# Kernel optimization log

Hardware: AMD Instinct MI355X
Metric: run time of the kernel (lower is better)

## Reference

```python
import jax, jax.numpy as jnp
import numpy as np

B, N, C, H, R = 64, 197, 768, 12, 24  # batch, tokens (196 patches + cls), dim, heads, lora rank
D = C // H  # head_dim = 64


def make_rel_index(ws=(14, 14)):
    Wh, Ww = ws
    coords = np.stack(np.meshgrid(np.arange(Wh), np.arange(Ww), indexing='ij'))  # [2,Wh,Ww]
    cf = coords.reshape(2, -1)
    rel = (cf[:, :, None] - cf[:, None, :]).transpose(1, 2, 0).astype(np.int64)
    rel[:, :, 0] += Wh - 1
    rel[:, :, 1] += Ww - 1
    rel[:, :, 0] *= 2 * Ww - 1
    num_rel = (2 * Wh - 1) * (2 * Ww - 1) + 3
    idx = np.zeros((Wh * Ww + 1,) * 2, dtype=np.int32)
    idx[1:, 1:] = rel.sum(-1)
    idx[0, :] = num_rel - 3
    idx[:, 0] = num_rel - 2
    idx[0, 0] = num_rel - 1
    return idx


def setup_inputs() -> dict:
    key = jax.random.key(0)
    ks = jax.random.split(key, 16)
    s = 0.02
    # 1D rotary table over 196 patch positions, interleaved pairs over head_dim
    pos = np.arange(N - 1, dtype=np.float32)
    inv_freq = 1.0 / (10000.0 ** (np.arange(0, D, 2, dtype=np.float32) / D))  # [D/2]
    ang = np.repeat(pos[:, None] * inv_freq[None, :], 2, axis=-1)  # [196, 64]
    return {
        'x': jax.random.normal(ks[0], (B, N, C), jnp.float32),
        'qkv_w': jax.random.normal(ks[1], (3 * C, C), jnp.float32) * s,
        'q_bias': jax.random.normal(ks[2], (C,), jnp.float32) * s,
        'v_bias': jax.random.normal(ks[3], (C,), jnp.float32) * s,
        'lora_q_a': jax.random.normal(ks[4], (R, C), jnp.float32) * s,
        'lora_q_b': jax.random.normal(ks[5], (C, R), jnp.float32) * s,
        'lora_k_a': jax.random.normal(ks[6], (R, C), jnp.float32) * s,
        'lora_k_b': jax.random.normal(ks[7], (C, R), jnp.float32) * s,
        'lora_v_a': jax.random.normal(ks[8], (R, C), jnp.float32) * s,
        'lora_v_b': jax.random.normal(ks[9], (C, R), jnp.float32) * s,
        'rel_table': jax.random.normal(ks[10], (732, H), jnp.float32) * s,
        'rope_cos': jnp.asarray(np.cos(ang)),
        'rope_sin': jnp.asarray(np.sin(ang)),
        'proj_w': jax.random.normal(ks[11], (C, C), jnp.float32) * s,
        'proj_b': jax.random.normal(ks[12], (C,), jnp.float32) * s,
        'rel_index': jnp.asarray(make_rel_index((14, 14))),
    }


def _rope(t, cos, sin):
    # t: [B,H,M,D]; cos/sin: [M,D]; EVA rotate_half over interleaved pairs
    tp = t.reshape(t.shape[:-1] + (D // 2, 2))
    rot = jnp.stack((-tp[..., 1], tp[..., 0]), axis=-1).reshape(t.shape)
    return t * cos + rot * sin


def reference(x, qkv_w, q_bias, v_bias, lora_q_a, lora_q_b, lora_k_a, lora_k_b,
              lora_v_a, lora_v_b, rel_table, rope_cos, rope_sin, proj_w, proj_b, rel_index):
    b, n, c = x.shape
    h = rel_table.shape[1]
    d = c // h
    scale = d ** -0.5
    bias = jnp.concatenate([q_bias, jnp.zeros_like(v_bias), v_bias])
    qkv = x @ qkv_w.T + bias  # [B,N,3C]
    lora = jnp.concatenate([(x @ lora_q_a.T) @ lora_q_b.T,
                            (x @ lora_k_a.T) @ lora_k_b.T,
                            (x @ lora_v_a.T) @ lora_v_b.T], axis=-1)
    qkv = (qkv + lora).reshape(b, n, 3, h, d).transpose(2, 0, 3, 1, 4)  # [3,B,H,N,D]
    q, k, v = qkv[0], qkv[1], qkv[2]
    # rope on non-cls tokens only
    q = jnp.concatenate([q[:, :, :1], _rope(q[:, :, 1:], rope_cos, rope_sin)], axis=2)
    k = jnp.concatenate([k[:, :, :1], _rope(k[:, :, 1:], rope_cos, rope_sin)], axis=2)
    attn = jnp.einsum('bhqd,bhkd->bhqk', (q * scale).astype(jnp.float32), k.astype(jnp.float32))
    rpb = rel_table[rel_index.reshape(-1)].reshape(n, n, h).transpose(2, 0, 1)  # [H,N,N]
    attn = attn + rpb[None].astype(attn.dtype)
    attn = jax.nn.softmax(attn, axis=-1).astype(x.dtype)
    out = jnp.einsum('bhqk,bhkd->bhqd', attn, v).transpose(0, 2, 1, 3).reshape(b, n, c)
    return out @ proj_w.T + proj_b
```

## Files before the change

### kernel.cpp

```cpp
#include <hip/hip_runtime.h>
#include <stdint.h>

typedef __bf16 bf16x8 __attribute__((ext_vector_type(8)));
typedef short short8 __attribute__((ext_vector_type(8)));
typedef float f32x4 __attribute__((ext_vector_type(4)));
typedef float f32x4v __attribute__((ext_vector_type(4)));
typedef unsigned short u16x4 __attribute__((ext_vector_type(4)));

#define DEV static __device__ __forceinline__

DEV float b2f(unsigned short u) {
    union { float f; unsigned v; } x; x.v = ((unsigned)u) << 16; return x.f;
}
DEV unsigned short f2b(float f) {
    union { float f; unsigned v; } x; x.f = f;
    unsigned r = x.v + 0x7fffu + ((x.v >> 16) & 1u);
    return (unsigned short)(r >> 16);
}
DEV f32x4 zero4() { f32x4 z; z[0]=0.f; z[1]=0.f; z[2]=0.f; z[3]=0.f; return z; }

#define MFMA16(a, b, c) __builtin_amdgcn_mfma_f32_16x16x32_bf16(a, b, c, 0, 0, 0)

DEV void gload16(const unsigned short* g, unsigned short* l) {
    __builtin_amdgcn_global_load_lds(
        (const __attribute__((address_space(1))) void*)g,
        (__attribute__((address_space(3))) void*)l,
        16, 0, 0);
}

__global__ __launch_bounds__(256)
void prep_kernel(const float* __restrict__ x, unsigned short* __restrict__ xb,
                 const float* __restrict__ pw, unsigned short* __restrict__ pwb,
                 const float* __restrict__ qkvw,
                 const float* __restrict__ qa, const float* __restrict__ qbb,
                 const float* __restrict__ ka, const float* __restrict__ kb,
                 const float* __restrict__ va, const float* __restrict__ vbb,
                 unsigned short* __restrict__ W,
                 const float* __restrict__ rtab, const int* __restrict__ ridx,
                 float* __restrict__ rpb)
{
    const int S0 = 9682944 / 4;
    const int S1 = 589824 / 4;
    const int S2 = 2304 * 768;
    const int S3 = 12 * 197 * 224;
    const int total = S0 + S1 + S2 + S3;
    for (int i = blockIdx.x * 256 + threadIdx.x; i < total; i += gridDim.x * 256) {
        if (i < S0) {
            f32x4v v = *(const f32x4v*)(x + (size_t)i * 4);
            u16x4 o;
            #pragma unroll
            for (int j = 0; j < 4; ++j) o[j] = f2b(v[j]);
            *(u16x4*)(xb + (size_t)i * 4) = o;
        } else if (i < S0 + S1) {
            const int k = i - S0;
            f32x4v v = *(const f32x4v*)(pw + (size_t)k * 4);
            u16x4 o;
            #pragma unroll
            for (int j = 0; j < 4; ++j) o[j] = f2b(v[j]);
            *(u16x4*)(pwb + (size_t)k * 4) = o;
        } else if (i < S0 + S1 + S2) {
            const int idx = i - S0 - S1;
            const int o = idx / 768;
            const int c = idx - o * 768;
            const int sec = o / 768;
            const int ol = o - sec * 768;
            const float* a_ = (sec == 0) ? qa : (sec == 1 ? ka : va);
            const float* b_ = (sec == 0) ? qbb : (sec == 1 ? kb : vbb);
            float acc = qkvw[idx];
            #pragma unroll
            for (int r = 0; r < 24; ++r)
                acc += b_[ol * 24 + r] * a_[r * 768 + c];
            W[idx] = f2b(acc);
        } else {
            const int idx = i - S0 - S1 - S2;
            const int h = idx / (197 * 224);
            const int rem = idx - h * 197 * 224;
            const int qq = rem / 224;
            const int kk = rem - qq * 224;
            float v = 0.f;
            if (kk < 197) v = rtab[ridx[qq * 197 + kk] * 12 + h];
            rpb[idx] = v;
        }
    }
}

template<int EPI>
__global__ __launch_bounds__(256, 2)
void gemm_bt(const unsigned short* __restrict__ A, const unsigned short* __restrict__ Bw,
             int M, int Nout, int ntn,
             const float* __restrict__ qb, const float* __restrict__ vb,
             const float* __restrict__ rcos, const float* __restrict__ rsin,
             unsigned short* __restrict__ oq, unsigned short* __restrict__ ok,
             unsigned short* __restrict__ ov,
             const float* __restrict__ pb, float* __restrict__ o2)
{
    constexpr int K = 768, TK = 24;
    __shared__ __align__(16) unsigned short lA[3][128 * 32];
    __shared__ __align__(16) unsigned short lB[3][128 * 32];
    const int tid = threadIdx.x;
    const int lane = tid & 63, wave = tid >> 6;

    const int nwg = gridDim.x;
    const int qq_ = nwg >> 3, rr_ = nwg & 7;
    const int xcd = blockIdx.x & 7, orig8 = blockIdx.x >> 3;
    const int wgid = (xcd < rr_ ? xcd * (qq_ + 1) : rr_ * (qq_ + 1) + (xcd - rr_) * qq_) + orig8;
    const int mt = wgid / ntn, nt = wgid - mt * ntn;
    const int m0 = mt * 128, n0 = nt * 128;
    const int wm = (wave >> 1) * 64, wn = (wave & 1) * 64;

    int srow[2], sunit[2];
    #pragma unroll
    for (int j = 0; j < 2; ++j) {
        const int P = wave * 2048 + j * 1024 + lane * 16;
        const int L = P ^ (((P >> 7) & 7) << 4);
        srow[j] = L >> 6;
        sunit[j] = (L >> 4) & 3;
    }

    const int laneA = lane & 15, laneQ = lane >> 4;
    int aoff[4], boff[4];
    #pragma unroll
    for (int i = 0; i < 4; ++i) {
        int lb = (wm + i * 16 + laneA) * 64 + laneQ * 16;
        aoff[i] = (lb ^ (((lb >> 7) & 7) << 4)) >> 1;
        lb = (wn + i * 16 + laneA) * 64 + laneQ * 16;
        boff[i] = (lb ^ (((lb >> 7) & 7) << 4)) >> 1;
    }

    f32x4 acc[4][4];
    #pragma unroll
    for (int i = 0; i < 4; ++i)
        #pragma unroll
        for (int j = 0; j < 4; ++j) acc[i][j] = zero4();

    auto stage = [&](int kt, int bsel) {
        const int k0 = kt << 5;
        #pragma unroll
        for (int j = 0; j < 2; ++j) {
            int gr = m0 + srow[j]; if (gr > M - 1) gr = M - 1;
            gload16(A + (size_t)gr * K + k0 + sunit[j] * 8,
                    (unsigned short*)lA[bsel] + wave * 1024 + j * 512);
        }
        #pragma unroll
        for (int j = 0; j < 2; ++j) {
            const int br = n0 + srow[j];
            gload16(Bw + (size_t)br * K + k0 + sunit[j] * 8,
                    (unsigned short*)lB[bsel] + wave * 1024 + j * 512);
        }
    };

    stage(0, 0);
    stage(1, 1);
    asm volatile("s_waitcnt vmcnt(4)" ::: "memory");
    __builtin_amdgcn_s_barrier();

    #pragma unroll
    for (int t = 0; t < TK; ++t) {
        if (t + 2 < TK) stage(t + 2, (t + 2) % 3);
        const unsigned short* aT = (const unsigned short*)lA[t % 3];
        const unsigned short* bT = (const unsigned short*)lB[t % 3];
        bf16x8 af[4], bfr[4];
        #pragma unroll
        for (int i = 0; i < 4; ++i) af[i] = *(const bf16x8*)(aT + aoff[i]);
        #pragma unroll
        for (int i = 0; i < 4; ++i) bfr[i] = *(const bf16x8*)(bT + boff[i]);
        #pragma unroll
        for (int mi = 0; mi < 4; ++mi)
            #pragma unroll
            for (int ni = 0; ni < 4; ++ni)
                acc[mi][ni] = MFMA16(af[mi], bfr[ni], acc[mi][ni]);
        if (t + 1 < TK) {
            if (t + 2 < TK) asm volatile("s_waitcnt vmcnt(4)" ::: "memory");
            else            asm volatile("s_waitcnt vmcnt(0)" ::: "memory");
            __builtin_amdgcn_s_barrier();
        }
    }

    #pragma unroll
    for (int mi = 0; mi < 4; ++mi) {
        #pragma unroll
        for (int j = 0; j < 4; ++j) {
            const int m = m0 + wm + mi * 16 + (lane >> 4) * 4 + j;
            const bool mv = (m < M);
            int b_ = 0, n = 0;
            if constexpr (EPI == 1) { b_ = m / 197; n = m - b_ * 197; }
            #pragma unroll
            for (int ni = 0; ni < 4; ++ni) {
                const int o = n0 + wn + ni * 16 + laneA;
                float val = acc[mi][ni][j];
                if constexpr (EPI == 1) {
                    const int sec = o / 768;
                    const int oc = o - sec * 768;
                    const int d = oc & 63;
                    if (sec == 0) val += qb[oc];
                    else if (sec == 2) val += vb[oc];
                    if (sec < 2 && n > 0) {
                        const float part = __shfl_xor(val, 1, 64);
                        const float co = rcos[(n - 1) * 64 + d];
                        const float si = rsin[(n - 1) * 64 + d];
                        val = val * co + ((o & 1) ? part : -part) * si;
                    }
                    if (sec == 0) val *= 0.125f;
                    if (mv) {
                        const int h = oc >> 6;
                        unsigned short* dst = (sec == 0) ? oq : (sec == 1 ? ok : ov);
                        dst[((size_t)(b_ * 12 + h) * 197 + n) * 64 + d] = f2b(val);
                    }
                } else {
                    val += pb[o];
                    if (mv) o2[(size_t)m * Nout + o] = val;
                }
            }
        }
    }
}

__global__ __launch_bounds__(256)
void attn_kernel(const unsigned short* __restrict__ qs, const unsigned short* __restrict__ ksrc,
                 const unsigned short* __restrict__ vsrc, const float* __restrict__ rpb,
                 unsigned short* __restrict__ aout)
{
    __shared__ __align__(16) unsigned short Pl[64 * 232];
    __shared__ __align__(16) unsigned short Vt[64 * 232];
    __shared__ float inv_s[64];
    const int chunk = blockIdx.x;
    const int h = blockIdx.y;
    const int b = blockIdx.z;
    const int tid = threadIdx.x, lane = tid & 63, wave = tid >> 6;
    const size_t base = ((size_t)(b * 12 + h)) * 197 * 64;
    const unsigned short* q = qs + base;
    const unsigned short* kp = ksrc + base;
    const unsigned short* vp = vsrc + base;

    if (tid < 224) {
        const int kc = tid;
        if (kc < 197) {
            #pragma unroll
            for (int d0 = 0; d0 < 8; ++d0) {
                short8 vv = *(const short8*)(vp + kc * 64 + d0 * 8);
                #pragma unroll
                for (int i = 0; i < 8; ++i)
                    Vt[(d0 * 8 + i) * 232 + kc] = (unsigned short)vv[i];
            }
        } else {
            #pragma unroll
            for (int dd = 0; dd < 64; ++dd) Vt[dd * 232 + kc] = 0;
        }
    }

    const int laneA = lane & 15;
    const int laneK = (lane >> 4) * 8;
    const int q0 = chunk * 64 + wave * 16;

    int qr = q0 + laneA; if (qr > 196) qr = 196;
    const bf16x8 qf0 = *(const bf16x8*)(q + qr * 64 + laneK);
    const bf16x8 qf1 = *(const bf16x8*)(q + qr * 64 + 32 + laneK);

    f32x4 s[13];
    #pragma unroll
    for (int kt = 0; kt < 13; ++kt) {
        int kr = kt * 16 + laneA; if (kr > 196) kr = 196;
        const bf16x8 kf0 = *(const bf16x8*)(kp + kr * 64 + laneK);
        const bf16x8 kf1 = *(const bf16x8*)(kp + kr * 64 + 32 + laneK);
        f32x4 c = zero4();
        c = MFMA16(qf0, kf0, c);
        c = MFMA16(qf1, kf1, c);
        s[kt] = c;
    }

    const int rowb = (lane >> 4) * 4;
    float mx[4] = {-1e30f, -1e30f, -1e30f, -1e30f};
    #pragma unroll
    for (int kt = 0; kt < 13; ++kt) {
        const int kc = kt * 16 + laneA;
        #pragma unroll
        for (int j = 0; j < 4; ++j) {
            int qg = q0 + rowb + j; if (qg > 196) qg = 196;
            float v = s[kt][j] + rpb[((size_t)h * 197 + qg) * 224 + kc];
            if (kc > 196) v = -1e30f;
            s[kt][j] = v;
            mx[j] = fmaxf(mx[j], v);
        }
    }
    #pragma unroll
    for (int off = 1; off < 16; off <<= 1)
        #pragma unroll
        for (int j = 0; j < 4; ++j) mx[j] = fmaxf(mx[j], __shfl_xor(mx[j], off, 64));
    float sm[4] = {0.f, 0.f, 0.f, 0.f};
    #pragma unroll
    for (int kt = 0; kt < 13; ++kt)
        #pragma unroll
        for (int j = 0; j < 4; ++j) {
            const float e = __expf(s[kt][j] - mx[j]);
            s[kt][j] = e;
            sm[j] += e;
        }
    #pragma unroll
    for (int off = 1; off < 16; off <<= 1)
        #pragma unroll
        for (int j = 0; j < 4; ++j) sm[j] += __shfl_xor(sm[j], off, 64);
    if (laneA == 0) {
        #pragma unroll
        for (int j = 0; j < 4; ++j) inv_s[wave * 16 + rowb + j] = 1.0f / sm[j];
    }
    #pragma unroll
    for (int kt = 0; kt < 13; ++kt) {
        const int kc = kt * 16 + laneA;
        #pragma unroll
        for (int j = 0; j < 4; ++j) {
            const int lr = wave * 16 + rowb + j;
            Pl[lr * 232 + kc] = (kc <= 196) ? f2b(s[kt][j]) : (unsigned short)0;
        }
    }
    #pragma unroll
    for (int j = 0; j < 4; ++j)
        Pl[(wave * 16 + rowb + j) * 232 + 208 + laneA] = 0;

    __syncthreads();

    f32x4 oacc[4];
    #pragma unroll
    for (int i = 0; i < 4; ++i) oacc[i] = zero4();
    #pragma unroll
    for (int ks2 = 0; ks2 < 7; ++ks2) {
        const bf16x8 pf = *(const bf16x8*)(Pl + (wave * 16 + laneA) * 232 + ks2 * 32 + laneK);
        #pragma unroll
        for (int ni = 0; ni < 4; ++ni) {
            const bf16x8 vf = *(const bf16x8*)(Vt + (ni * 16 + laneA) * 232 + ks2 * 32 + laneK);
            oacc[ni] = MFMA16(pf, vf, oacc[ni]);
        }
    }
    #pragma unroll
    for (int ni = 0; ni < 4; ++ni)
        #pragma unroll
        for (int j = 0; j < 4; ++j) {
            const int lq = wave * 16 + rowb + j;
            const int qg = chunk * 64 + lq;
            if (qg < 197) {
                const int d = ni * 16 + laneA;
                const float val = oacc[ni][j] * inv_s[lq];
                aout[((size_t)b * 197 + qg) * 768 + h * 64 + d] = f2b(val);
            }
        }
}

extern "C" void kernel_launch(void* const* d_in, const int* in_sizes, int n_in,
                              void* d_out, int out_size, void* d_ws, size_t ws_size,
                              hipStream_t stream)
{
    const float* x    = (const float*)d_in[0];
    const float* qkvw = (const float*)d_in[1];
    const float* qb   = (const float*)d_in[2];
    const float* vb   = (const float*)d_in[3];
    const float* lqa  = (const float*)d_in[4];
    const float* lqb  = (const float*)d_in[5];
    const float* lka  = (const float*)d_in[6];
    const float* lkb  = (const float*)d_in[7];
    const float* lva  = (const float*)d_in[8];
    const float* lvb  = (const float*)d_in[9];
    const float* rtab = (const float*)d_in[10];
    const float* rcos = (const float*)d_in[11];
    const float* rsin = (const float*)d_in[12];
    const float* pw   = (const float*)d_in[13];
    const float* pb   = (const float*)d_in[14];
    const int* ridx   = (const int*)d_in[15];

    const int M = 64 * 197;
    const size_t XSZ = (size_t)M * 768;
    const size_t QSZ = (size_t)64 * 12 * 197 * 64;

    char* ws = (char*)d_ws;
    unsigned short* xb   = (unsigned short*)ws;
    unsigned short* pwb  = xb + XSZ;
    unsigned short* Weff = pwb + (size_t)768 * 768;
    unsigned short* qsb  = Weff + (size_t)2304 * 768;
    unsigned short* ksb  = qsb + QSZ;
    unsigned short* vsb  = ksb + QSZ;
    float* rpb           = (float*)(vsb + QSZ);
    unsigned short* aout = (unsigned short*)(rpb + (size_t)12 * 197 * 224);

    prep_kernel<<<2048, 256, 0, stream>>>(x, xb, pw, pwb, qkvw,
                                          lqa, lqb, lka, lkb, lva, lvb, Weff,
                                          rtab, ridx, rpb);
    gemm_bt<1><<<99 * 18, 256, 0, stream>>>(xb, Weff, M, 2304, 18,
                                            qb, vb, rcos, rsin, qsb, ksb, vsb,
                                            nullptr, nullptr);
    attn_kernel<<<dim3(4, 12, 64), 256, 0, stream>>>(qsb, ksb, vsb, rpb, aout);
    gemm_bt<2><<<99 * 6, 256, 0, stream>>>(aout, pwb, M, 768, 6,
                                           nullptr, nullptr, nullptr, nullptr,
                                           nullptr, nullptr, nullptr,
                                           pb, (float*)d_out);
}
```

Baseline: 239.8 us.

## Replace LDS-staged GEMM with direct global-to-register double-buffered loads

Both projection GEMMs now skip shared memory entirely. Each lane loads its MFMA operand fragments straight from global memory into a two-deep register buffer, and the launch bound rises to allow three blocks per CU. This removes the LDS staging, swizzle math and per-step barriers. In exchange, operand rows are re-read by multiple waves instead of being shared through LDS, which raises cache and global traffic and gives less coalesced access.

```diff
diff --git a/kernel.cpp b/kernel.cpp
--- a/kernel.cpp
+++ b/kernel.cpp
@@ -20,13 +20,6 @@
 DEV f32x4 zero4() { f32x4 z; z[0]=0.f; z[1]=0.f; z[2]=0.f; z[3]=0.f; return z; }
 
 #define MFMA16(a, b, c) __builtin_amdgcn_mfma_f32_16x16x32_bf16(a, b, c, 0, 0, 0)
-
-DEV void gload16(const unsigned short* g, unsigned short* l) {
-    __builtin_amdgcn_global_load_lds(
-        (const __attribute__((address_space(1))) void*)g,
-        (__attribute__((address_space(3))) void*)l,
-        16, 0, 0);
-}
 
 __global__ __launch_bounds__(256)
 void prep_kernel(const float* __restrict__ x, unsigned short* __restrict__ xb,
@@ -85,18 +78,16 @@
 }
 
 template<int EPI>
-__global__ __launch_bounds__(256, 2)
-void gemm_bt(const unsigned short* __restrict__ A, const unsigned short* __restrict__ Bw,
-             int M, int Nout, int ntn,
-             const float* __restrict__ qb, const float* __restrict__ vb,
-             const float* __restrict__ rcos, const float* __restrict__ rsin,
-             unsigned short* __restrict__ oq, unsigned short* __restrict__ ok,
-             unsigned short* __restrict__ ov,
-             const float* __restrict__ pb, float* __restrict__ o2)
+__global__ __launch_bounds__(256, 3)
+void gemm_nolds(const unsigned short* __restrict__ A, const unsigned short* __restrict__ Bw,
+                int M, int Nout, int ntn,
+                const float* __restrict__ qb, const float* __restrict__ vb,
+                const float* __restrict__ rcos, const float* __restrict__ rsin,
+                unsigned short* __restrict__ oq, unsigned short* __restrict__ ok,
+                unsigned short* __restrict__ ov,
+                const float* __restrict__ pb, float* __restrict__ o2)
 {
     constexpr int K = 768, TK = 24;
-    __shared__ __align__(16) unsigned short lA[3][128 * 32];
-    __shared__ __align__(16) unsigned short lB[3][128 * 32];
     const int tid = threadIdx.x;
     const int lane = tid & 63, wave = tid >> 6;
 
@@ -108,23 +99,19 @@
     const int m0 = mt * 128, n0 = nt * 128;
     const int wm = (wave >> 1) * 64, wn = (wave & 1) * 64;
 
-    int srow[2], sunit[2];
-    #pragma unroll
-    for (int j = 0; j < 2; ++j) {
-        const int P = wave * 2048 + j * 1024 + lane * 16;
-        const int L = P ^ (((P >> 7) & 7) << 4);
-        srow[j] = L >> 6;
-        sunit[j] = (L >> 4) & 3;
-    }
-
     const int laneA = lane & 15, laneQ = lane >> 4;
-    int aoff[4], boff[4];
+
+    const unsigned short* ap[4];
+    const unsigned short* bp[4];
     #pragma unroll
     for (int i = 0; i < 4; ++i) {
-        int lb = (wm + i * 16 + laneA) * 64 + laneQ * 16;
-        aoff[i] = (lb ^ (((lb >> 7) & 7) << 4)) >> 1;
-        lb = (wn + i * 16 + laneA) * 64 + laneQ * 16;
-        boff[i] = (lb ^ (((lb >> 7) & 7) << 4)) >> 1;
+        int ar = m0 + wm + i * 16 + laneA; if (ar > M - 1) ar = M - 1;
+        ap[i] = A + (size_t)ar * K + laneQ * 8;
+    }
+    #pragma unroll
+    for (int i = 0; i < 4; ++i) {
+        const int br = n0 + wn + i * 16 + laneA;
+        bp[i] = Bw + (size_t)br * K + laneQ * 8;
     }
 
     f32x4 acc[4][4];
@@ -133,54 +120,35 @@
         #pragma unroll
         for (int j = 0; j < 4; ++j) acc[i][j] = zero4();
 
-    auto stage = [&](int kt, int bsel) {
-        const int k0 = kt << 5;
-        #pragma unroll
-        for (int j = 0; j < 2; ++j) {
-            int gr = m0 + srow[j]; if (gr > M - 1) gr = M - 1;
-            gload16(A + (size_t)gr * K + k0 + sunit[j] * 8,
-                    (unsigned short*)lA[bsel] + wave * 1024 + j * 512);
-        }
-        #pragma unroll
-        for (int j = 0; j < 2; ++j) {
-            const int br = n0 + srow[j];
-            gload16(Bw + (size_t)br * K + k0 + sunit[j] * 8,
-                    (unsigned short*)lB[bsel] + wave * 1024 + j * 512);
-        }
-    };
-
-    stage(0, 0);
-    stage(1, 1);
-    asm volatile("s_waitcnt vmcnt(4)" ::: "memory");
-    __builtin_amdgcn_s_barrier();
+    bf16x8 abuf[2][4], bbuf[2][4];
+    #pragma unroll
+    for (int i = 0; i < 4; ++i) {
+        abuf[0][i] = *(const bf16x8*)(ap[i]);
+        bbuf[0][i] = *(const bf16x8*)(bp[i]);
+    }
 
     #pragma unroll
     for (int t = 0; t < TK; ++t) {
-        if (t + 2 < TK) stage(t + 2, (t + 2) % 3);
-        const unsigned short* aT = (const unsigned short*)lA[t % 3];
-        const unsigned short* bT = (const unsigned short*)lB[t % 3];
-        bf16x8 af[4], bfr[4];
-        #pragma unroll
-        for (int i = 0; i < 4; ++i) af[i] = *(const bf16x8*)(aT + aoff[i]);
-        #pragma unroll
-        for (int i = 0; i < 4; ++i) bfr[i] = *(const bf16x8*)(bT + boff[i]);
+        const int c = t & 1, nx = c ^ 1;
+        if (t + 1 < TK) {
+            #pragma unroll
+            for (int i = 0; i < 4; ++i) {
+                abuf[nx][i] = *(const bf16x8*)(ap[i] + (t + 1) * 32);
+                bbuf[nx][i] = *(const bf16x8*)(bp[i] + (t + 1) * 32);
+            }
+        }
         #pragma unroll
         for (int mi = 0; mi < 4; ++mi)
             #pragma unroll
             for (int ni = 0; ni < 4; ++ni)
-                acc[mi][ni] = MFMA16(af[mi], bfr[ni], acc[mi][ni]);
-        if (t + 1 < TK) {
-            if (t + 2 < TK) asm volatile("s_waitcnt vmcnt(4)" ::: "memory");
-            else            asm volatile("s_waitcnt vmcnt(0)" ::: "memory");
-            __builtin_amdgcn_s_barrier();
-        }
+                acc[mi][ni] = MFMA16(abuf[c][mi], bbuf[c][ni], acc[mi][ni]);
     }
 
     #pragma unroll
     for (int mi = 0; mi < 4; ++mi) {
         #pragma unroll
         for (int j = 0; j < 4; ++j) {
-            const int m = m0 + wm + mi * 16 + (lane >> 4) * 4 + j;
+            const int m = m0 + wm + mi * 16 + laneQ * 4 + j;
             const bool mv = (m < M);
             int b_ = 0, n = 0;
             if constexpr (EPI == 1) { b_ = m / 197; n = m - b_ * 197; }
@@ -382,12 +350,12 @@
     prep_kernel<<<2048, 256, 0, stream>>>(x, xb, pw, pwb, qkvw,
                                           lqa, lqb, lka, lkb, lva, lvb, Weff,
                                           rtab, ridx, rpb);
-    gemm_bt<1><<<99 * 18, 256, 0, stream>>>(xb, Weff, M, 2304, 18,
-                                            qb, vb, rcos, rsin, qsb, ksb, vsb,
-                                            nullptr, nullptr);
+    gemm_nolds<1><<<99 * 18, 256, 0, stream>>>(xb, Weff, M, 2304, 18,
+                                               qb, vb, rcos, rsin, qsb, ksb, vsb,
+                                               nullptr, nullptr);
     attn_kernel<<<dim3(4, 12, 64), 256, 0, stream>>>(qsb, ksb, vsb, rpb, aout);
-    gemm_bt<2><<<99 * 6, 256, 0, stream>>>(aout, pwb, M, 768, 6,
-                                           nullptr, nullptr, nullptr, nullptr,
-                                           nullptr, nullptr, nullptr,
-                                           pb, (float*)d_out);
-}
+    gemm_nolds<2><<<99 * 6, 256, 0, stream>>>(aout, pwb, M, 768, 6,
+                                              nullptr, nullptr, nullptr, nullptr,
+                                              nullptr, nullptr, nullptr,
+                                              pb, (float*)d_out);
+}
```

Measured after the change: 387.0 us. 1.61x slower.

## Load GEMM B operand directly into registers and raise occupancy

Applied to the files above, without the earlier changes.

Both GEMMs stop staging the weight (B) tile through shared memory. Each wave now reads its B fragments straight from global memory into a double-buffered register array, while the A tile keeps the triple-buffered LDS path, and the vmcnt waits are adjusted to match. Halving LDS per block allows launch bounds of 4 blocks per SM instead of 2, aiming for more latency hiding. The trade-off is that waves sharing the same B columns now fetch them separately, which adds global/L2 traffic, and the per-lane global loads are less coalesced than the LDS staging.

```diff
diff --git a/kernel.cpp b/kernel.cpp
--- a/kernel.cpp
+++ b/kernel.cpp
@@ -85,18 +85,17 @@
 }
 
 template<int EPI>
-__global__ __launch_bounds__(256, 2)
-void gemm_bt(const unsigned short* __restrict__ A, const unsigned short* __restrict__ Bw,
-             int M, int Nout, int ntn,
-             const float* __restrict__ qb, const float* __restrict__ vb,
-             const float* __restrict__ rcos, const float* __restrict__ rsin,
-             unsigned short* __restrict__ oq, unsigned short* __restrict__ ok,
-             unsigned short* __restrict__ ov,
-             const float* __restrict__ pb, float* __restrict__ o2)
+__global__ __launch_bounds__(256, 4)
+void gemm_hyb(const unsigned short* __restrict__ A, const unsigned short* __restrict__ Bw,
+              int M, int Nout, int ntn,
+              const float* __restrict__ qb, const float* __restrict__ vb,
+              const float* __restrict__ rcos, const float* __restrict__ rsin,
+              unsigned short* __restrict__ oq, unsigned short* __restrict__ ok,
+              unsigned short* __restrict__ ov,
+              const float* __restrict__ pb, float* __restrict__ o2)
 {
     constexpr int K = 768, TK = 24;
     __shared__ __align__(16) unsigned short lA[3][128 * 32];
-    __shared__ __align__(16) unsigned short lB[3][128 * 32];
     const int tid = threadIdx.x;
     const int lane = tid & 63, wave = tid >> 6;
 
@@ -118,13 +117,18 @@
     }
 
     const int laneA = lane & 15, laneQ = lane >> 4;
-    int aoff[4], boff[4];
+    int aoff[4];
     #pragma unroll
     for (int i = 0; i < 4; ++i) {
         int lb = (wm + i * 16 + laneA) * 64 + laneQ * 16;
         aoff[i] = (lb ^ (((lb >> 7) & 7) << 4)) >> 1;
-        lb = (wn + i * 16 + laneA) * 64 + laneQ * 16;
-        boff[i] = (lb ^ (((lb >> 7) & 7) << 4)) >> 1;
+    }
+
+    const unsigned short* bp[4];
+    #pragma unroll
+    for (int i = 0; i < 4; ++i) {
+        const int br = n0 + wn + i * 16 + laneA;
+        bp[i] = Bw + (size_t)br * K + laneQ * 8;
     }
 
     f32x4 acc[4][4];
@@ -133,7 +137,7 @@
         #pragma unroll
         for (int j = 0; j < 4; ++j) acc[i][j] = zero4();
 
-    auto stage = [&](int kt, int bsel) {
+    auto stageA = [&](int kt, int bsel) {
         const int k0 = kt << 5;
         #pragma unroll
         for (int j = 0; j < 2; ++j) {
@@ -141,36 +145,37 @@
             gload16(A + (size_t)gr * K + k0 + sunit[j] * 8,
                     (unsigned short*)lA[bsel] + wave * 1024 + j * 512);
         }
-        #pragma unroll
-        for (int j = 0; j < 2; ++j) {
-            const int br = n0 + srow[j];
-            gload16(Bw + (size_t)br * K + k0 + sunit[j] * 8,
-                    (unsigned short*)lB[bsel] + wave * 1024 + j * 512);
-        }
     };
 
-    stage(0, 0);
-    stage(1, 1);
-    asm volatile("s_waitcnt vmcnt(4)" ::: "memory");
+    bf16x8 bbuf[2][4];
+
+    stageA(0, 0);
+    #pragma unroll
+    for (int i = 0; i < 4; ++i) bbuf[0][i] = *(const bf16x8*)(bp[i]);
+    stageA(1, 1);
+    asm volatile("s_waitcnt vmcnt(2)" ::: "memory");
     __builtin_amdgcn_s_barrier();
 
     #pragma unroll
     for (int t = 0; t < TK; ++t) {
-        if (t + 2 < TK) stage(t + 2, (t + 2) % 3);
+        const int c = t & 1, nx = c ^ 1;
+        if (t + 1 < TK) {
+            #pragma unroll
+            for (int i = 0; i < 4; ++i)
+                bbuf[nx][i] = *(const bf16x8*)(bp[i] + (t + 1) * 32);
+        }
+        if (t + 2 < TK) stageA(t + 2, (t + 2) % 3);
         const unsigned short* aT = (const unsigned short*)lA[t % 3];
-        const unsigned short* bT = (const unsigned short*)lB[t % 3];
-        bf16x8 af[4], bfr[4];
+        bf16x8 af[4];
         #pragma unroll
         for (int i = 0; i < 4; ++i) af[i] = *(const bf16x8*)(aT + aoff[i]);
         #pragma unroll
-        for (int i = 0; i < 4; ++i) bfr[i] = *(const bf16x8*)(bT + boff[i]);
-        #pragma unroll
         for (int mi = 0; mi < 4; ++mi)
             #pragma unroll
             for (int ni = 0; ni < 4; ++ni)
-                acc[mi][ni] = MFMA16(af[mi], bfr[ni], acc[mi][ni]);
+                acc[mi][ni] = MFMA16(af[mi], bbuf[c][ni], acc[mi][ni]);
         if (t + 1 < TK) {
-            if (t + 2 < TK) asm volatile("s_waitcnt vmcnt(4)" ::: "memory");
+            if (t + 2 < TK) asm volatile("s_waitcnt vmcnt(2)" ::: "memory");
             else            asm volatile("s_waitcnt vmcnt(0)" ::: "memory");
             __builtin_amdgcn_s_barrier();
         }
@@ -180,7 +185,7 @@
     for (int mi = 0; mi < 4; ++mi) {
         #pragma unroll
         for (int j = 0; j < 4; ++j) {
-            const int m = m0 + wm + mi * 16 + (lane >> 4) * 4 + j;
+            const int m = m0 + wm + mi * 16 + laneQ * 4 + j;
             const bool mv = (m < M);
             int b_ = 0, n = 0;
             if constexpr (EPI == 1) { b_ = m / 197; n = m - b_ * 197; }
@@ -382,12 +387,12 @@
     prep_kernel<<<2048, 256, 0, stream>>>(x, xb, pw, pwb, qkvw,
                                           lqa, lqb, lka, lkb, lva, lvb, Weff,
                                           rtab, ridx, rpb);
-    gemm_bt<1><<<99 * 18, 256, 0, stream>>>(xb, Weff, M, 2304, 18,
-                                            qb, vb, rcos, rsin, qsb, ksb, vsb,
-                                            nullptr, nullptr);
+    gemm_hyb<1><<<99 * 18, 256, 0, stream>>>(xb, Weff, M, 2304, 18,
+                                             qb, vb, rcos, rsin, qsb, ksb, vsb,
+                                             nullptr, nullptr);
     attn_kernel<<<dim3(4, 12, 64), 256, 0, stream>>>(qsb, ksb, vsb, rpb, aout);
-    gemm_bt<2><<<99 * 6, 256, 0, stream>>>(aout, pwb, M, 768, 6,
-                                           nullptr, nullptr, nullptr, nullptr,
-                                           nullptr, nullptr, nullptr,
-                                           pb, (float*)d_out);
-}
+    gemm_hyb<2><<<99 * 6, 256, 0, stream>>>(aout, pwb, M, 768, 6,
+                                            nullptr, nullptr, nullptr, nullptr,
+                                            nullptr, nullptr, nullptr,
+                                            pb, (float*)d_out);
+}
```

New measurement: 285.3 us. 1.19x slower.

## Replace GEMM with 256x256-tile, 8-wave kernel using staggered LDS staging

Applied to the files above, without the earlier changes.

Replaces the 128x128 three-stage GEMM with a 512-thread kernel that computes 256x256 output tiles. It steps through K in 64-wide slices with double-buffered LDS. The A and B half-tile loads are spread across four sub-steps that alternate with MFMA bursts, using barriers and s_setprio to stagger memory and compute. The aim is more data reuse per LDS load and fewer K iterations. The trade-offs are about 128KB of LDS per block, a larger accumulator footprint, and far fewer blocks, especially for the 768-wide projection GEMM, which may leave CUs idle.

```diff
diff --git a/kernel.cpp b/kernel.cpp
--- a/kernel.cpp
+++ b/kernel.cpp
@@ -85,108 +85,149 @@
 }
 
 template<int EPI>
-__global__ __launch_bounds__(256, 2)
-void gemm_bt(const unsigned short* __restrict__ A, const unsigned short* __restrict__ Bw,
-             int M, int Nout, int ntn,
-             const float* __restrict__ qb, const float* __restrict__ vb,
-             const float* __restrict__ rcos, const float* __restrict__ rsin,
-             unsigned short* __restrict__ oq, unsigned short* __restrict__ ok,
-             unsigned short* __restrict__ ov,
-             const float* __restrict__ pb, float* __restrict__ o2)
+__global__ __launch_bounds__(512, 2)
+void gemm8p(const unsigned short* __restrict__ A, const unsigned short* __restrict__ Bw,
+            int M, int Nout, int ntn,
+            const float* __restrict__ qb, const float* __restrict__ vb,
+            const float* __restrict__ rcos, const float* __restrict__ rsin,
+            unsigned short* __restrict__ oq, unsigned short* __restrict__ ok,
+            unsigned short* __restrict__ ov,
+            const float* __restrict__ pb, float* __restrict__ o2)
 {
-    constexpr int K = 768, TK = 24;
-    __shared__ __align__(16) unsigned short lA[3][128 * 32];
-    __shared__ __align__(16) unsigned short lB[3][128 * 32];
+    constexpr int K = 768, TKT = 12;
+    __shared__ __align__(16) unsigned short lA[2][2][128 * 64];
+    __shared__ __align__(16) unsigned short lB[2][2][128 * 64];
     const int tid = threadIdx.x;
-    const int lane = tid & 63, wave = tid >> 6;
+    const int lane = tid & 63;
+    const int wave = tid >> 6;
+    const int wm_ = wave >> 2;
+    const int wn_ = wave & 3;
 
     const int nwg = gridDim.x;
     const int qq_ = nwg >> 3, rr_ = nwg & 7;
     const int xcd = blockIdx.x & 7, orig8 = blockIdx.x >> 3;
     const int wgid = (xcd < rr_ ? xcd * (qq_ + 1) : rr_ * (qq_ + 1) + (xcd - rr_) * qq_) + orig8;
     const int mt = wgid / ntn, nt = wgid - mt * ntn;
-    const int m0 = mt * 128, n0 = nt * 128;
-    const int wm = (wave >> 1) * 64, wn = (wave & 1) * 64;
-
-    int srow[2], sunit[2];
+    const int m0 = mt * 256, n0 = nt * 256;
+
+    int srow[2], scol[2];
     #pragma unroll
     for (int j = 0; j < 2; ++j) {
-        const int P = wave * 2048 + j * 1024 + lane * 16;
+        const int P = (j * 512 + tid) * 16;
         const int L = P ^ (((P >> 7) & 7) << 4);
-        srow[j] = L >> 6;
-        sunit[j] = (L >> 4) & 3;
+        srow[j] = L >> 7;
+        scol[j] = (L & 127) >> 1;
     }
 
     const int laneA = lane & 15, laneQ = lane >> 4;
-    int aoff[4], boff[4];
-    #pragma unroll
-    for (int i = 0; i < 4; ++i) {
-        int lb = (wm + i * 16 + laneA) * 64 + laneQ * 16;
-        aoff[i] = (lb ^ (((lb >> 7) & 7) << 4)) >> 1;
-        lb = (wn + i * 16 + laneA) * 64 + laneQ * 16;
-        boff[i] = (lb ^ (((lb >> 7) & 7) << 4)) >> 1;
-    }
-
-    f32x4 acc[4][4];
-    #pragma unroll
-    for (int i = 0; i < 4; ++i)
+
+    int aoffs[8][2], boffs[4][2];
+    #pragma unroll
+    for (int mi = 0; mi < 8; ++mi)
+        #pragma unroll
+        for (int kk = 0; kk < 2; ++kk) {
+            const int b = (mi * 16 + laneA) * 128 + (kk * 4 + laneQ) * 16;
+            aoffs[mi][kk] = (b ^ (((b >> 7) & 7) << 4)) >> 1;
+        }
+    #pragma unroll
+    for (int ni = 0; ni < 4; ++ni)
+        #pragma unroll
+        for (int kk = 0; kk < 2; ++kk) {
+            const int b = ((wn_ & 1) * 64 + ni * 16 + laneA) * 128 + (kk * 4 + laneQ) * 16;
+            boffs[ni][kk] = (b ^ (((b >> 7) & 7) << 4)) >> 1;
+        }
+
+    f32x4 acc[8][4];
+    #pragma unroll
+    for (int i = 0; i < 8; ++i)
         #pragma unroll
         for (int j = 0; j < 4; ++j) acc[i][j] = zero4();
 
-    auto stage = [&](int kt, int bsel) {
-        const int k0 = kt << 5;
+    auto stageA = [&](int kt, int half) {
+        unsigned short* dst = &lA[kt & 1][half][0];
         #pragma unroll
         for (int j = 0; j < 2; ++j) {
-            int gr = m0 + srow[j]; if (gr > M - 1) gr = M - 1;
-            gload16(A + (size_t)gr * K + k0 + sunit[j] * 8,
-                    (unsigned short*)lA[bsel] + wave * 1024 + j * 512);
-        }
+            int gr = m0 + half * 128 + srow[j]; if (gr > M - 1) gr = M - 1;
+            gload16(A + (size_t)gr * K + kt * 64 + scol[j], dst + (size_t)(j * 512 + tid) * 8);
+        }
+    };
+    auto stageB = [&](int kt, int half) {
+        unsigned short* dst = &lB[kt & 1][half][0];
         #pragma unroll
         for (int j = 0; j < 2; ++j) {
-            const int br = n0 + srow[j];
-            gload16(Bw + (size_t)br * K + k0 + sunit[j] * 8,
-                    (unsigned short*)lB[bsel] + wave * 1024 + j * 512);
+            const int br = n0 + half * 128 + srow[j];
+            gload16(Bw + (size_t)br * K + kt * 64 + scol[j], dst + (size_t)(j * 512 + tid) * 8);
         }
     };
 
-    stage(0, 0);
-    stage(1, 1);
+    stageB(0, 0); stageB(0, 1); stageA(0, 0); stageA(0, 1);
+    stageB(1, 0); stageB(1, 1);
     asm volatile("s_waitcnt vmcnt(4)" ::: "memory");
     __builtin_amdgcn_s_barrier();
-
-    #pragma unroll
-    for (int t = 0; t < TK; ++t) {
-        if (t + 2 < TK) stage(t + 2, (t + 2) % 3);
-        const unsigned short* aT = (const unsigned short*)lA[t % 3];
-        const unsigned short* bT = (const unsigned short*)lB[t % 3];
-        bf16x8 af[4], bfr[4];
-        #pragma unroll
-        for (int i = 0; i < 4; ++i) af[i] = *(const bf16x8*)(aT + aoff[i]);
-        #pragma unroll
-        for (int i = 0; i < 4; ++i) bfr[i] = *(const bf16x8*)(bT + boff[i]);
-        #pragma unroll
-        for (int mi = 0; mi < 4; ++mi)
-            #pragma unroll
-            for (int ni = 0; ni < 4; ++ni)
-                acc[mi][ni] = MFMA16(af[mi], bfr[ni], acc[mi][ni]);
-        if (t + 1 < TK) {
-            if (t + 2 < TK) asm volatile("s_waitcnt vmcnt(4)" ::: "memory");
-            else            asm volatile("s_waitcnt vmcnt(0)" ::: "memory");
+    asm volatile("" ::: "memory");
+
+    bf16x8 bfr[4][2];
+
+    #pragma unroll
+    for (int kt = 0; kt < TKT; ++kt) {
+        const unsigned short* Ab = &lA[kt & 1][wm_][0];
+        const unsigned short* Bb = &lB[kt & 1][wn_ >> 1][0];
+        #pragma unroll
+        for (int q = 0; q < 4; ++q) {
+            bf16x8 af[2][2];
+            if (q == 0) {
+                #pragma unroll
+                for (int ni = 0; ni < 4; ++ni)
+                    #pragma unroll
+                    for (int kk = 0; kk < 2; ++kk)
+                        bfr[ni][kk] = *(const bf16x8*)(Bb + boffs[ni][kk]);
+            }
+            #pragma unroll
+            for (int dm = 0; dm < 2; ++dm)
+                #pragma unroll
+                for (int kk = 0; kk < 2; ++kk)
+                    af[dm][kk] = *(const bf16x8*)(Ab + aoffs[q * 2 + dm][kk]);
+            if (q == 0)      { if (kt + 1 < TKT) stageA(kt + 1, 0); }
+            else if (q == 1) { if (kt + 1 < TKT) stageA(kt + 1, 1); }
+            else if (q == 2) { if (kt + 2 < TKT) stageB(kt + 2, 0); }
+            else             { if (kt + 2 < TKT) stageB(kt + 2, 1); }
             __builtin_amdgcn_s_barrier();
-        }
-    }
-
-    #pragma unroll
-    for (int mi = 0; mi < 4; ++mi) {
+            asm volatile("s_waitcnt lgkmcnt(0)" ::: "memory");
+            __builtin_amdgcn_sched_barrier(0);
+            __builtin_amdgcn_s_setprio(1);
+            #pragma unroll
+            for (int kk = 0; kk < 2; ++kk)
+                #pragma unroll
+                for (int dm = 0; dm < 2; ++dm)
+                    #pragma unroll
+                    for (int ni = 0; ni < 4; ++ni)
+                        acc[q * 2 + dm][ni] = MFMA16(af[dm][kk], bfr[ni][kk], acc[q * 2 + dm][ni]);
+            __builtin_amdgcn_s_setprio(0);
+            if (q == 3) {
+                if (kt + 1 < TKT) {
+                    if (kt + 2 < TKT) asm volatile("s_waitcnt vmcnt(4)" ::: "memory");
+                    else              asm volatile("s_waitcnt vmcnt(0)" ::: "memory");
+                    __builtin_amdgcn_s_barrier();
+                    asm volatile("" ::: "memory");
+                }
+            } else {
+                __builtin_amdgcn_s_barrier();
+                asm volatile("" ::: "memory");
+            }
+        }
+    }
+
+    #pragma unroll
+    for (int mi = 0; mi < 8; ++mi) {
         #pragma unroll
         for (int j = 0; j < 4; ++j) {
-            const int m = m0 + wm + mi * 16 + (lane >> 4) * 4 + j;
+            const int m = m0 + wm_ * 128 + mi * 16 + laneQ * 4 + j;
             const bool mv = (m < M);
             int b_ = 0, n = 0;
             if constexpr (EPI == 1) { b_ = m / 197; n = m - b_ * 197; }
             #pragma unroll
             for (int ni = 0; ni < 4; ++ni) {
-                const int o = n0 + wn + ni * 16 + laneA;
+                const int o = n0 + wn_ * 64 + ni * 16 + laneA;
                 float val = acc[mi][ni][j];
                 if constexpr (EPI == 1) {
                     const int sec = o / 768;
@@ -382,12 +423,13 @@
     prep_kernel<<<2048, 256, 0, stream>>>(x, xb, pw, pwb, qkvw,
                                           lqa, lqb, lka, lkb, lva, lvb, Weff,
                                           rtab, ridx, rpb);
-    gemm_bt<1><<<99 * 18, 256, 0, stream>>>(xb, Weff, M, 2304, 18,
-                                            qb, vb, rcos, rsin, qsb, ksb, vsb,
-                                            nullptr, nullptr);
+    const int MT = (M + 255) / 256;
+    gemm8p<1><<<MT * 9, 512, 0, stream>>>(xb, Weff, M, 2304, 9,
+                                          qb, vb, rcos, rsin, qsb, ksb, vsb,
+                                          nullptr, nullptr);
     attn_kernel<<<dim3(4, 12, 64), 256, 0, stream>>>(qsb, ksb, vsb, rpb, aout);
-    gemm_bt<2><<<99 * 6, 256, 0, stream>>>(aout, pwb, M, 768, 6,
-                                           nullptr, nullptr, nullptr, nullptr,
-                                           nullptr, nullptr, nullptr,
-                                           pb, (float*)d_out);
-}
+    gemm8p<2><<<MT * 3, 512, 0, stream>>>(aout, pwb, M, 768, 3,
+                                          nullptr, nullptr, nullptr, nullptr,
+                                          nullptr, nullptr, nullptr,
+                                          pb, (float*)d_out);
+}
```

Result: slower. 252.3 us (+5.2%).
